# Performance work log

Hardware: AMD Instinct MI355X
Metric: run time of the kernel (lower is better)

The kernel has to match this reference:

```python
import jax, jax.numpy as jnp
import numpy as np

N = 100000
E = 640000
D = 128
L = 3
B = 128
OUT = 10


def setup_inputs() -> dict:
    key = jax.random.key(0)
    ks = jax.random.split(key, 8)
    x = jax.random.normal(ks[0], (N, D), dtype=jnp.float32)
    edge_index = jax.random.randint(ks[1], (2, E), 0, N, dtype=jnp.int64)
    batch = jnp.sort(jax.random.randint(ks[2], (N,), 0, B, dtype=jnp.int64))
    # per-layer GCNConv weights (in==hidden==D so they stack) and biases
    Ws = jax.random.normal(ks[3], (L, D, D), dtype=jnp.float32) / np.sqrt(D)
    bs = jnp.zeros((L, D), dtype=jnp.float32)
    # MLP head: single Linear(hidden -> out), norm=None
    W_mlp = jax.random.normal(ks[4], (D, OUT), dtype=jnp.float32) / np.sqrt(D)
    b_mlp = jnp.zeros((OUT,), dtype=jnp.float32)
    return {"x": x, "edge_index": edge_index, "batch": batch,
            "Ws": Ws, "bs": bs, "W_mlp": W_mlp, "b_mlp": b_mlp}


def reference(x, edge_index, batch, Ws, bs, W_mlp, b_mlp):
    n = x.shape[0]
    # --- GCN normalization (PyG gcn_norm with self-loops, edge_weight=1) ---
    loop = jnp.arange(n, dtype=edge_index.dtype)
    src = jnp.concatenate([edge_index[0], loop])  # message sources (x_j)
    dst = jnp.concatenate([edge_index[1], loop])  # aggregation targets
    deg = jax.ops.segment_sum(jnp.ones_like(dst, dtype=x.dtype), dst, num_segments=n)
    dinv = jnp.where(deg > 0, jax.lax.rsqrt(jnp.maximum(deg, 1.0)), 0.0)
    norm = dinv[src] * dinv[dst]  # [E+N]

    def gcn_conv(h, W, b):
        hw = h @ W  # [N, D] dense transform
        msg = hw[src] * norm[:, None]  # gather + scale [E+N, D]
        agg = jax.ops.segment_sum(msg, dst, num_segments=n)  # scatter-add
        return agg + b

    h = x
    for l in range(Ws.shape[0]):
        h = jax.nn.relu(gcn_conv(h, Ws[l], bs[l]))

    # global add pool over graphs
    pooled = jax.ops.segment_sum(h, batch, num_segments=B)  # [B, D]
    # MLP head (single linear, no norm/act)
    return pooled @ W_mlp + b_mlp
```

## Files before the change

### kernel.cpp

```cpp
#include <hip/hip_runtime.h>
#include <hip/hip_bf16.h>

#define N_NODES 100000
#define N_EDGES 640000
#define DIM 128
#define N_LAYERS 3
#define N_GRAPHS 128
#define N_OUT 10
#define SCAN_BLK 1024
#define N_SCAN_BLKS ((N_NODES + SCAN_BLK - 1) / SCAN_BLK)
#define PCHUNK 128
#define NXCD 8
#define RNODES (N_NODES / NXCD)
#define R_EST 98304
#define BE 1000
#define RK 40
#define GEMM_GRID 782
#define SMASK 0x1FFFF

typedef _Float16 h4 __attribute__((ext_vector_type(4)));
typedef _Float16 h2 __attribute__((ext_vector_type(2)));
typedef _Float16 h8 __attribute__((ext_vector_type(8)));
typedef float f32x4 __attribute__((ext_vector_type(4)));


__global__ __launch_bounds__(256) void bucket_edges(const int* __restrict__ ei,
                                                    int* __restrict__ rangeCur,
                                                    unsigned int* __restrict__ staging) {
    __shared__ int hist[NXCD];
    __shared__ int base[NXCD];
    const int e0 = blockIdx.x * BE;
    if (threadIdx.x < NXCD) hist[threadIdx.x] = 0;
    __syncthreads();

    unsigned int pk[4]; int r[4];
    #pragma unroll
    for (int k = 0; k < 4; ++k) {
        int e = e0 + threadIdx.x + k * 256;
        if (e < e0 + BE) {
            int s = ei[e];
            int d = ei[N_EDGES + e];
            r[k] = d / RNODES;
            pk[k] = (unsigned int)s | ((unsigned int)(d - r[k] * RNODES) << 17);
            atomicAdd(&hist[r[k]], 1);
        } else r[k] = -1;
    }
    __syncthreads();
    if (threadIdx.x < NXCD) base[threadIdx.x] = atomicAdd(&rangeCur[threadIdx.x], hist[threadIdx.x]);
    __syncthreads();
    if (threadIdx.x < NXCD) hist[threadIdx.x] = 0;
    __syncthreads();

    #pragma unroll
    for (int k = 0; k < 4; ++k) {
        if (r[k] >= 0) {
            int idx = base[r[k]] + atomicAdd(&hist[r[k]], 1);
            staging[(size_t)r[k] * R_EST + idx] = pk[k];
        }
    }
}


__global__ __launch_bounds__(256) void hist_pinned(const unsigned int* __restrict__ staging,
                                                   const int* __restrict__ rangeCur,
                                                   int* __restrict__ cnt) {
    const int g = blockIdx.x & (NXCD - 1);
    const int b = blockIdx.x >> 3;
    const int n = rangeCur[g];
    const unsigned int* st = staging + (size_t)g * R_EST;
    const int dbase = g * RNODES;
    for (int j = b * 256 + threadIdx.x; j < n; j += RK * 256)
        atomicAdd(&cnt[dbase + (st[j] >> 17)], 1);
}


__global__ void scan1(const int* __restrict__ cnt, int* __restrict__ off, int* __restrict__ bsum,
                      float* __restrict__ dinv) {
    __shared__ int tmp[256];
    int base = blockIdx.x * SCAN_BLK + threadIdx.x * 4;
    int c[4];
    #pragma unroll
    for (int k = 0; k < 4; ++k) c[k] = (base + k < N_NODES) ? cnt[base + k] : 0;
    #pragma unroll
    for (int k = 0; k < 4; ++k)
        if (base + k < N_NODES) dinv[base + k] = rsqrtf((float)(c[k] + 1));
    int tot = c[0] + c[1] + c[2] + c[3];
    tmp[threadIdx.x] = tot;
    __syncthreads();
    int val = tot;
    for (int d = 1; d < 256; d <<= 1) {
        int add = (threadIdx.x >= d) ? tmp[threadIdx.x - d] : 0;
        __syncthreads();
        val += add;
        tmp[threadIdx.x] = val;
        __syncthreads();
    }
    int ex = val - tot;
    int e1 = ex + c[0], e2 = e1 + c[1], e3 = e2 + c[2];
    if (base + 0 < N_NODES) off[base + 0] = ex;
    if (base + 1 < N_NODES) off[base + 1] = e1;
    if (base + 2 < N_NODES) off[base + 2] = e2;
    if (base + 3 < N_NODES) off[base + 3] = e3;
    if (threadIdx.x == 255) bsum[blockIdx.x] = val;
}

__global__ void scan2(int* __restrict__ bsum) {
    __shared__ int tmp[128];
    int t = threadIdx.x;
    int v = (t < N_SCAN_BLKS) ? bsum[t] : 0;
    int own = v;
    tmp[t] = v;
    __syncthreads();
    for (int d = 1; d < 128; d <<= 1) {
        int add = (t >= d) ? tmp[t - d] : 0;
        __syncthreads();
        v += add;
        tmp[t] = v;
        __syncthreads();
    }
    if (t < N_SCAN_BLKS) bsum[t] = v - own;
}

__global__ void scan3(int* __restrict__ off, const int* __restrict__ bsum) {
    int i = blockIdx.x * blockDim.x + threadIdx.x;
    if (i < N_NODES) off[i] += bsum[i / SCAN_BLK];
    if (i == 0) off[N_NODES] = N_EDGES;
}


__global__ __launch_bounds__(256) void fill_pinned(const unsigned int* __restrict__ staging,
                                                   const int* __restrict__ rangeCur,
                                                   const int* __restrict__ off,
                                                   int* __restrict__ cursor,
                                                   int* __restrict__ csr_src) {
    const int g = blockIdx.x & (NXCD - 1);
    const int b = blockIdx.x >> 3;
    const int n = rangeCur[g];
    const unsigned int* st = staging + (size_t)g * R_EST;
    const int dbase = g * RNODES;
    for (int j = b * 256 + threadIdx.x; j < n; j += RK * 256) {
        unsigned int v = st[j];
        int d = dbase + (int)(v >> 17);
        int pos = off[d] + atomicAdd(&cursor[d], 1);
        csr_src[pos] = (int)(v & SMASK);
    }
}


__global__ void wt_prep(const float* __restrict__ Ws, _Float16* __restrict__ wt) {
    int t = blockIdx.x * blockDim.x + threadIdx.x;
    if (t >= N_LAYERS * DIM * 32) return;
    int u = t & 31;
    int n = (t >> 5) & 127;
    int l = t >> 12;
    const float* W = Ws + (size_t)l * DIM * DIM;
    int k0 = u * 4;
    h4 v;
    v.x = (_Float16)W[(k0 + 0) * DIM + n];
    v.y = (_Float16)W[(k0 + 1) * DIM + n];
    v.z = (_Float16)W[(k0 + 2) * DIM + n];
    v.w = (_Float16)W[(k0 + 3) * DIM + n];
    int du = u ^ (n & 31);
    ((h4*)wt)[(size_t)l * 4096 + n * 32 + du] = v;
}


template<typename TIN>
__global__ __launch_bounds__(256) void gemm_mfma(const TIN* __restrict__ in,
                                                 const _Float16* __restrict__ wt,
                                                 const float* __restrict__ dinv,
                                                 _Float16* __restrict__ out) {
    __shared__ __align__(16) h4 Wl[4096];
    __shared__ __align__(16) h4 Hl[2048];
    {
        const float4* src = (const float4*)wt;
        float4* dst = (float4*)Wl;
        #pragma unroll
        for (int i = 0; i < 8; ++i) dst[threadIdx.x + i * 256] = src[threadIdx.x + i * 256];
    }

    const int wave = threadIdx.x >> 6;
    const int lane = threadIdx.x & 63;
    const int row = lane & 15;
    const int g   = lane >> 4;
    const int hrow = wave * 16 + row;

    for (int c0 = blockIdx.x * 64; c0 < N_NODES; c0 += GEMM_GRID * 64) {
        __syncthreads();

        if constexpr (sizeof(TIN) == 2) {
            #pragma unroll
            for (int it = 0; it < 4; ++it) {
                int i = threadIdx.x + it * 256;
                int r = i >> 4, u8 = i & 15;
                int rs = c0 + r; if (rs > N_NODES - 1) rs = N_NODES - 1;
                h8 v = *(const h8*)((const _Float16*)in + (size_t)rs * DIM + u8 * 8);
                ((h8*)Hl)[r * 16 + (u8 ^ (r & 15))] = v;
            }
        } else {
            #pragma unroll
            for (int it = 0; it < 8; ++it) {
                int j = threadIdx.x + it * 256;
                int r = j >> 5, u4 = j & 31;
                int rs = c0 + r; if (rs > N_NODES - 1) rs = N_NODES - 1;
                float4 f = *(const float4*)((const float*)in + (size_t)rs * DIM + u4 * 4);
                h4 v; v.x = (_Float16)f.x; v.y = (_Float16)f.y;
                v.z = (_Float16)f.z; v.w = (_Float16)f.w;
                Hl[r * 32 + ((u4 >> 1) ^ (r & 15)) * 2 + (u4 & 1)] = v;
            }
        }
        __syncthreads();

        f32x4 acc[8] = {};
        #pragma unroll
        for (int kc = 0; kc < 8; ++kc) {
            const h4 bfrag = Hl[hrow * 32 + ((kc * 2 + (g >> 1)) ^ (hrow & 15)) * 2 + (g & 1)];
            const int u = kc * 4 + g;
            #pragma unroll
            for (int nb = 0; nb < 8; ++nb) {
                const int n = nb * 16 + row;
                acc[nb] = __builtin_amdgcn_mfma_f32_16x16x16f16(Wl[n * 32 + (u ^ (n & 31))],
                                                                bfrag, acc[nb], 0, 0, 0);
            }
        }

        const int m = c0 + hrow;
        if (m < N_NODES) {
            const float di = dinv[m];
            _Float16* orow = out + (size_t)m * DIM;
            #pragma unroll
            for (int nb = 0; nb < 8; ++nb) {
                h4 v;
                v.x = (_Float16)(acc[nb].x * di); v.y = (_Float16)(acc[nb].y * di);
                v.z = (_Float16)(acc[nb].z * di); v.w = (_Float16)(acc[nb].w * di);
                ((h4*)orow)[nb * 4 + g] = v;
            }
        }
    }
}


__global__ __launch_bounds__(256) void gather_agg(const _Float16* __restrict__ hw,
                                                  const float* __restrict__ dinv,
                                                  const int* __restrict__ off,
                                                  const int* __restrict__ csr_src,
                                                  const float* __restrict__ bias,
                                                  _Float16* __restrict__ hout) {
    const int i = (blockIdx.x * blockDim.x + threadIdx.x) >> 6;
    if (i >= N_NODES) return;
    const int lane = threadIdx.x & 63;
    const int grp    = lane >> 3;
    const int stream = grp & 3;
    const int half   = grp >> 2;
    const int sub    = lane & 7;
    const int idx8   = half * 8 + sub;
    const h8* hw8 = (const h8*)hw;

    const int beg = off[i], end = off[i + 1];
    h8 acc = {};

    if (stream == 3) acc = hw8[(size_t)i * 16 + idx8];

    int j = beg + stream;
    for (; j + 4 < end; j += 8) {
        int s0 = csr_src[j];
        int s1 = csr_src[j + 4];
        h8 v0 = hw8[(size_t)s0 * 16 + idx8];
        h8 v1 = hw8[(size_t)s1 * 16 + idx8];
        #pragma unroll
        for (int p = 0; p < 4; ++p) {
            ((h2*)&acc)[p] += ((h2*)&v0)[p];
            ((h2*)&acc)[p] += ((h2*)&v1)[p];
        }
    }
    for (; j < end; j += 4) {
        int s0 = csr_src[j];
        h8 v0 = hw8[(size_t)s0 * 16 + idx8];
        #pragma unroll
        for (int p = 0; p < 4; ++p) ((h2*)&acc)[p] += ((h2*)&v0)[p];
    }

    unsigned int* au = (unsigned int*)&acc;
    #pragma unroll
    for (int p = 0; p < 4; ++p) {
        unsigned int o = __shfl_xor(au[p], 8);
        h2 a = *(h2*)&au[p]; a += *(h2*)&o; au[p] = *(unsigned int*)&a;
        o = __shfl_xor(au[p], 16);
        h2 b = *(h2*)&au[p]; b += *(h2*)&o; au[p] = *(unsigned int*)&b;
    }

    if (stream == 0) {
        const float di = dinv[i];
        const float4 b0 = *(const float4*)&bias[half * 64 + sub * 8];
        const float4 b1 = *(const float4*)&bias[half * 64 + sub * 8 + 4];
        h8 v;
        v[0] = (_Float16)fmaxf((float)acc[0] * di + b0.x, 0.0f);
        v[1] = (_Float16)fmaxf((float)acc[1] * di + b0.y, 0.0f);
        v[2] = (_Float16)fmaxf((float)acc[2] * di + b0.z, 0.0f);
        v[3] = (_Float16)fmaxf((float)acc[3] * di + b0.w, 0.0f);
        v[4] = (_Float16)fmaxf((float)acc[4] * di + b1.x, 0.0f);
        v[5] = (_Float16)fmaxf((float)acc[5] * di + b1.y, 0.0f);
        v[6] = (_Float16)fmaxf((float)acc[6] * di + b1.z, 0.0f);
        v[7] = (_Float16)fmaxf((float)acc[7] * di + b1.w, 0.0f);
        ((h8*)hout)[(size_t)i * 16 + idx8] = v;
    }
}


__global__ __launch_bounds__(256) void pool_chunk(const _Float16* __restrict__ h,
                                                  const int* __restrict__ batch,
                                                  float* __restrict__ pooled) {
    const int base = blockIdx.x * PCHUNK;
    const int t = threadIdx.x;
    const int lane4 = t & 31;
    const int rgrp = t >> 5;
    const h4* hp = (const h4*)h;

    float a0 = 0.f, a1 = 0.f, a2 = 0.f, a3 = 0.f;
    int cur = -1;
    const int rend = (base + PCHUNK < N_NODES) ? base + PCHUNK : N_NODES;
    for (int r = base + rgrp; r < rend; r += 8) {
        int b = batch[r];
        if (b != cur) {
            if (cur >= 0) {
                float* pp = &pooled[cur * DIM + lane4 * 4];
                atomicAdd(pp + 0, a0); atomicAdd(pp + 1, a1);
                atomicAdd(pp + 2, a2); atomicAdd(pp + 3, a3);
            }
            cur = b; a0 = a1 = a2 = a3 = 0.f;
        }
        h4 v = hp[(size_t)r * 32 + lane4];
        a0 += (float)v.x; a1 += (float)v.y; a2 += (float)v.z; a3 += (float)v.w;
    }
    if (cur >= 0) {
        float* pp = &pooled[cur * DIM + lane4 * 4];
        atomicAdd(pp + 0, a0); atomicAdd(pp + 1, a1);
        atomicAdd(pp + 2, a2); atomicAdd(pp + 3, a3);
    }
}


__global__ void mlp_head(const float* __restrict__ pooled, const float* __restrict__ Wm,
                         const float* __restrict__ bm, float* __restrict__ out) {
    int t = blockIdx.x * blockDim.x + threadIdx.x;
    if (t >= N_GRAPHS * N_OUT) return;
    int b = t / N_OUT;
    int o = t % N_OUT;
    float acc = bm[o];
    #pragma unroll 8
    for (int k = 0; k < DIM; ++k) acc += pooled[b * DIM + k] * Wm[k * N_OUT + o];
    out[t] = acc;
}


extern "C" void kernel_launch(void* const* d_in, const int* in_sizes, int n_in,
                              void* d_out, int out_size, void* d_ws, size_t ws_size,
                              hipStream_t stream) {
    const float* x     = (const float*)d_in[0];
    const int*   ei    = (const int*)d_in[1];
    const int*   batch = (const int*)d_in[2];
    const float* Ws    = (const float*)d_in[3];
    const float* bs    = (const float*)d_in[4];
    const float* Wm    = (const float*)d_in[5];
    const float* bm    = (const float*)d_in[6];
    float* out = (float*)d_out;

    char* p = (char*)d_ws;
    int*          cnt      = (int*)p;          p += N_NODES * 4;
    int*          cursor   = (int*)p;          p += N_NODES * 4;
    int*          rangeCur = (int*)p;          p += 16 * 4;
    float*        dinv     = (float*)p;        p += N_NODES * 4;
    int*          csr_off  = (int*)p;          p += (N_NODES + 16) * 4;
    int*          bsum     = (int*)p;          p += 128 * 4;
    _Float16*     wt       = (_Float16*)p;     p += (size_t)N_LAYERS * DIM * DIM * 2;
    int*          csr_src  = (int*)p;          p += (size_t)N_EDGES * 4;
    unsigned int* staging  = (unsigned int*)p; p += (size_t)NXCD * R_EST * 4;
    _Float16*     bufA     = (_Float16*)p;     p += (size_t)N_NODES * DIM * 2;
    _Float16*     bufB     = (_Float16*)p;     p += (size_t)N_NODES * DIM * 2;
    float*        pooled   = (float*)p;        p += N_GRAPHS * DIM * 4;

    const int nnode_blk = (N_NODES + 255) / 256;

    hipMemsetAsync(cnt, 0, N_NODES * 8 + 16 * 4, stream);
    hipMemsetAsync(pooled, 0, N_GRAPHS * DIM * 4, stream);

    bucket_edges<<<N_EDGES / BE, 256, 0, stream>>>(ei, rangeCur, staging);
    wt_prep<<<(N_LAYERS * DIM * 32 + 255) / 256, 256, 0, stream>>>(Ws, wt);

    hist_pinned<<<NXCD * RK, 256, 0, stream>>>(staging, rangeCur, cnt);

    scan1<<<N_SCAN_BLKS, 256, 0, stream>>>(cnt, csr_off, bsum, dinv);
    scan2<<<1, 128, 0, stream>>>(bsum);
    scan3<<<nnode_blk, 256, 0, stream>>>(csr_off, bsum);

    fill_pinned<<<NXCD * RK, 256, 0, stream>>>(staging, rangeCur, csr_off, cursor, csr_src);

    const int gather_grid = (N_NODES * 64 + 255) / 256;
    for (int l = 0; l < N_LAYERS; ++l) {
        if (l == 0) gemm_mfma<float><<<GEMM_GRID, 256, 0, stream>>>(x, wt, dinv, bufA);
        else        gemm_mfma<_Float16><<<GEMM_GRID, 256, 0, stream>>>(bufB, wt + (size_t)l * DIM * DIM, dinv, bufA);
        gather_agg<<<gather_grid, 256, 0, stream>>>(bufA, dinv, csr_off, csr_src, bs + l * DIM, bufB);
    }

    pool_chunk<<<(N_NODES + PCHUNK - 1) / PCHUNK, 256, 0, stream>>>(bufB, batch, pooled);
    mlp_head<<<(N_GRAPHS * N_OUT + 255) / 256, 256, 0, stream>>>(pooled, Wm, bm, out);
}
```

Baseline: 291.1 us.

## Fuse neighbor aggregation with next layer's MFMA GEMM per node tile

Adds a fused kernel that aggregates CSR neighbors for a 128-node tile into shared memory (with bias, relu and dinv scaling), then immediately runs the next layer's fp16 MFMA transform and writes the prescaled output. Layers 1 and 2 use this instead of a separate gather kernel plus GEMM kernel, so the intermediate activations no longer round-trip through global memory and two launches go away. In exchange the fused kernel uses 512-thread blocks with 64KB of shared memory, which may lower occupancy for the latency-bound gather. Each block also reloads the weight tile into shared memory, with far fewer blocks than the old persistent GEMM grid.

```diff
diff --git a/kernel.cpp b/kernel.cpp
--- a/kernel.cpp
+++ b/kernel.cpp
@@ -165,8 +165,7 @@
 }
 
 
-template<typename TIN>
-__global__ __launch_bounds__(256) void gemm_mfma(const TIN* __restrict__ in,
+__global__ __launch_bounds__(256) void gemm_mfma(const float* __restrict__ in,
                                                  const _Float16* __restrict__ wt,
                                                  const float* __restrict__ dinv,
                                                  _Float16* __restrict__ out) {
@@ -187,27 +186,15 @@
 
     for (int c0 = blockIdx.x * 64; c0 < N_NODES; c0 += GEMM_GRID * 64) {
         __syncthreads();
-
-        if constexpr (sizeof(TIN) == 2) {
-            #pragma unroll
-            for (int it = 0; it < 4; ++it) {
-                int i = threadIdx.x + it * 256;
-                int r = i >> 4, u8 = i & 15;
-                int rs = c0 + r; if (rs > N_NODES - 1) rs = N_NODES - 1;
-                h8 v = *(const h8*)((const _Float16*)in + (size_t)rs * DIM + u8 * 8);
-                ((h8*)Hl)[r * 16 + (u8 ^ (r & 15))] = v;
-            }
-        } else {
-            #pragma unroll
-            for (int it = 0; it < 8; ++it) {
-                int j = threadIdx.x + it * 256;
-                int r = j >> 5, u4 = j & 31;
-                int rs = c0 + r; if (rs > N_NODES - 1) rs = N_NODES - 1;
-                float4 f = *(const float4*)((const float*)in + (size_t)rs * DIM + u4 * 4);
-                h4 v; v.x = (_Float16)f.x; v.y = (_Float16)f.y;
-                v.z = (_Float16)f.z; v.w = (_Float16)f.w;
-                Hl[r * 32 + ((u4 >> 1) ^ (r & 15)) * 2 + (u4 & 1)] = v;
-            }
+        #pragma unroll
+        for (int it = 0; it < 8; ++it) {
+            int j = threadIdx.x + it * 256;
+            int r = j >> 5, u4 = j & 31;
+            int rs = c0 + r; if (rs > N_NODES - 1) rs = N_NODES - 1;
+            float4 f = *(const float4*)(in + (size_t)rs * DIM + u4 * 4);
+            h4 v; v.x = (_Float16)f.x; v.y = (_Float16)f.y;
+            v.z = (_Float16)f.z; v.w = (_Float16)f.w;
+            Hl[r * 32 + ((u4 >> 1) ^ (r & 15)) * 2 + (u4 & 1)] = v;
         }
         __syncthreads();
 
@@ -235,6 +222,118 @@
                 v.z = (_Float16)(acc[nb].z * di); v.w = (_Float16)(acc[nb].w * di);
                 ((h4*)orow)[nb * 4 + g] = v;
             }
+        }
+    }
+}
+
+
+__global__ __launch_bounds__(512) void fused_agg_gemm(const _Float16* __restrict__ hw_in,
+                                                      const float* __restrict__ dinv,
+                                                      const int* __restrict__ off,
+                                                      const int* __restrict__ csr_src,
+                                                      const float* __restrict__ bias,
+                                                      const _Float16* __restrict__ wt,
+                                                      _Float16* __restrict__ hw_out) {
+    __shared__ __align__(16) h4 Wl[4096];
+    __shared__ __align__(16) h4 Hl[4096];
+    {
+        const float4* src = (const float4*)wt;
+        float4* dst = (float4*)Wl;
+        #pragma unroll
+        for (int it = 0; it < 4; ++it) dst[threadIdx.x + it * 512] = src[threadIdx.x + it * 512];
+    }
+    __syncthreads();
+
+    const int wave = threadIdx.x >> 6;
+    const int lane = threadIdx.x & 63;
+    const int grp    = lane >> 3;
+    const int stream = grp & 3;
+    const int half   = grp >> 2;
+    const int sub    = lane & 7;
+    const int idx8   = half * 8 + sub;
+    const int c0 = blockIdx.x * 128;
+    const h8* hw8 = (const h8*)hw_in;
+
+    for (int n = 0; n < 16; ++n) {
+        const int r = wave * 16 + n;
+        const int i = c0 + r;
+        if (i >= N_NODES) break;
+        const int beg = off[i], end = off[i + 1];
+        h8 acc = {};
+        if (stream == 3) acc = hw8[(size_t)i * 16 + idx8];
+
+        int j = beg + stream;
+        for (; j + 4 < end; j += 8) {
+            int s0 = csr_src[j];
+            int s1 = csr_src[j + 4];
+            h8 v0 = hw8[(size_t)s0 * 16 + idx8];
+            h8 v1 = hw8[(size_t)s1 * 16 + idx8];
+            #pragma unroll
+            for (int p = 0; p < 4; ++p) {
+                ((h2*)&acc)[p] += ((h2*)&v0)[p];
+                ((h2*)&acc)[p] += ((h2*)&v1)[p];
+            }
+        }
+        for (; j < end; j += 4) {
+            int s0 = csr_src[j];
+            h8 v0 = hw8[(size_t)s0 * 16 + idx8];
+            #pragma unroll
+            for (int p = 0; p < 4; ++p) ((h2*)&acc)[p] += ((h2*)&v0)[p];
+        }
+
+        unsigned int* au = (unsigned int*)&acc;
+        #pragma unroll
+        for (int p = 0; p < 4; ++p) {
+            unsigned int o = __shfl_xor(au[p], 8);
+            h2 a = *(h2*)&au[p]; a += *(h2*)&o; au[p] = *(unsigned int*)&a;
+            o = __shfl_xor(au[p], 16);
+            h2 b = *(h2*)&au[p]; b += *(h2*)&o; au[p] = *(unsigned int*)&b;
+        }
+
+        if (stream == 0) {
+            const float di = dinv[i];
+            const float4 b0 = *(const float4*)&bias[half * 64 + sub * 8];
+            const float4 b1 = *(const float4*)&bias[half * 64 + sub * 8 + 4];
+            h8 v;
+            v[0] = (_Float16)fmaxf((float)acc[0] * di + b0.x, 0.0f);
+            v[1] = (_Float16)fmaxf((float)acc[1] * di + b0.y, 0.0f);
+            v[2] = (_Float16)fmaxf((float)acc[2] * di + b0.z, 0.0f);
+            v[3] = (_Float16)fmaxf((float)acc[3] * di + b0.w, 0.0f);
+            v[4] = (_Float16)fmaxf((float)acc[4] * di + b1.x, 0.0f);
+            v[5] = (_Float16)fmaxf((float)acc[5] * di + b1.y, 0.0f);
+            v[6] = (_Float16)fmaxf((float)acc[6] * di + b1.z, 0.0f);
+            v[7] = (_Float16)fmaxf((float)acc[7] * di + b1.w, 0.0f);
+            ((h8*)Hl)[r * 16 + (idx8 ^ (r & 15))] = v;
+        }
+    }
+
+    const int row = lane & 15;
+    const int g   = lane >> 4;
+    const int hrow = wave * 16 + row;
+    const int m = c0 + hrow;
+
+    f32x4 acc[8] = {};
+    #pragma unroll
+    for (int kc = 0; kc < 8; ++kc) {
+        const h4 bfrag = Hl[hrow * 32 + ((kc * 2 + (g >> 1)) ^ (hrow & 15)) * 2 + (g & 1)];
+        const int u = kc * 4 + g;
+        #pragma unroll
+        for (int nb = 0; nb < 8; ++nb) {
+            const int nn = nb * 16 + row;
+            acc[nb] = __builtin_amdgcn_mfma_f32_16x16x16f16(Wl[nn * 32 + (u ^ (nn & 31))],
+                                                            bfrag, acc[nb], 0, 0, 0);
+        }
+    }
+
+    if (m < N_NODES) {
+        const float di = dinv[m];
+        _Float16* orow = hw_out + (size_t)m * DIM;
+        #pragma unroll
+        for (int nb = 0; nb < 8; ++nb) {
+            h4 v;
+            v.x = (_Float16)(acc[nb].x * di); v.y = (_Float16)(acc[nb].y * di);
+            v.z = (_Float16)(acc[nb].z * di); v.w = (_Float16)(acc[nb].w * di);
+            ((h4*)orow)[nb * 4 + g] = v;
         }
     }
 }
@@ -395,12 +494,16 @@
 
     fill_pinned<<<NXCD * RK, 256, 0, stream>>>(staging, rangeCur, csr_off, cursor, csr_src);
 
+    const int fused_grid = (N_NODES + 127) / 128;
     const int gather_grid = (N_NODES * 64 + 255) / 256;
-    for (int l = 0; l < N_LAYERS; ++l) {
-        if (l == 0) gemm_mfma<float><<<GEMM_GRID, 256, 0, stream>>>(x, wt, dinv, bufA);
-        else        gemm_mfma<_Float16><<<GEMM_GRID, 256, 0, stream>>>(bufB, wt + (size_t)l * DIM * DIM, dinv, bufA);
-        gather_agg<<<gather_grid, 256, 0, stream>>>(bufA, dinv, csr_off, csr_src, bs + l * DIM, bufB);
-    }
+
+    gemm_mfma<<<GEMM_GRID, 256, 0, stream>>>(x, wt, dinv, bufA);
+    fused_agg_gemm<<<fused_grid, 512, 0, stream>>>(bufA, dinv, csr_off, csr_src,
+                                                   bs, wt + (size_t)1 * DIM * DIM, bufB);
+    fused_agg_gemm<<<fused_grid, 512, 0, stream>>>(bufB, dinv, csr_off, csr_src,
+                                                   bs + DIM, wt + (size_t)2 * DIM * DIM, bufA);
+    gather_agg<<<gather_grid, 256, 0, stream>>>(bufA, dinv, csr_off, csr_src,
+                                                bs + 2 * DIM, bufB);
 
     pool_chunk<<<(N_NODES + PCHUNK - 1) / PCHUNK, 256, 0, stream>>>(bufB, batch, pooled);
     mlp_head<<<(N_GRAPHS * N_OUT + 255) / 256, 256, 0, stream>>>(pooled, Wm, bm, out);
```

Result: slower. 327.5 us (+12.5%).
